# Kernel tuning notes

Measured on AMD Instinct MI355X. Metric: run time of the kernel, lower is better.

The kernel has to match this reference:

```python
import jax, jax.numpy as jnp
import numpy as np

N_NODES = 32768
N_EDGES = 262144
B = 64
FT_IN = 256
HID = 256
HEADS = 4
C = HID // HEADS
FT_OUT = 256
NEG_SLOPE = 0.2


def _lin(k, fi, fo):
    return jax.random.normal(k, (fi, fo), dtype=jnp.float32) / np.sqrt(fi)


def setup_inputs() -> dict:
    key = jax.random.key(0)
    ks = jax.random.split(key, 20)
    x = jax.random.normal(ks[0], (N_NODES, FT_IN), dtype=jnp.float32)
    edge_index = jax.random.randint(ks[1], (2, N_EDGES), 0, N_NODES, dtype=jnp.int64)
    batch = jnp.repeat(jnp.arange(B, dtype=jnp.int64), N_NODES // B)  # sorted segment ids
    return {
        "x": x,
        "edge_index": edge_index,
        "batch": batch,
        "batch_size": B,
        "W1l": _lin(ks[2], FT_IN, HID),
        "W1r": _lin(ks[3], FT_IN, HID),
        "a1": jax.random.normal(ks[4], (HEADS, C), dtype=jnp.float32) / np.sqrt(C),
        "b1": jnp.zeros((HID,), dtype=jnp.float32),
        "W2l": _lin(ks[5], HID, HID),
        "W2r": _lin(ks[6], HID, HID),
        "a2": jax.random.normal(ks[7], (HEADS, C), dtype=jnp.float32) / np.sqrt(C),
        "b2": jnp.zeros((HID,), dtype=jnp.float32),
        "Wm1": _lin(ks[8], HID, 4 * HID),
        "bm1": jnp.zeros((4 * HID,), dtype=jnp.float32),
        "Wm2": _lin(ks[9], 4 * HID, HID),
        "bm2": jnp.zeros((HID,), dtype=jnp.float32),
        "Wf": _lin(ks[10], HID, FT_OUT),
        "bf": jnp.zeros((FT_OUT,), dtype=jnp.float32),
    }


def gatv2_layer(x, src, dst, Wl, Wr, att, bias):
    """PyG GATv2Conv (concat=True, add_self_loops=True, eval-mode dropout)."""
    n = x.shape[0]
    h, c = att.shape
    xl = (x @ Wl).reshape(n, h, c)  # source-side transform (x_j)
    xr = (x @ Wr).reshape(n, h, c)  # target-side transform (x_i)
    loop = jnp.arange(n, dtype=src.dtype)
    s = jnp.concatenate([src, loop])
    d = jnp.concatenate([dst, loop])
    # e_ij = a^T LeakyReLU(Wl x_j + Wr x_i), per head
    e = jax.nn.leaky_relu(xl[s] + xr[d], NEG_SLOPE)  # [E+N, H, C]
    score = jnp.einsum('ehc,hc->eh', e, att)  # [E+N, H]
    # segment softmax over incoming edges of each dst node
    m = jax.ops.segment_max(score, d, num_segments=n)
    ex = jnp.exp(score - m[d])
    denom = jax.ops.segment_sum(ex, d, num_segments=n)
    alpha = ex / denom[d]  # self-loops guarantee denom > 0
    out = jax.ops.segment_sum(alpha[..., None] * xl[s], d, num_segments=n)
    return out.reshape(n, h * c) + bias


def _gelu(x):
    return jax.nn.gelu(x, approximate=False)


def reference(x, edge_index, batch, batch_size,
              W1l, W1r, a1, b1, W2l, W2r, a2, b2,
              Wm1, bm1, Wm2, bm2, Wf, bf):
    src, dst = edge_index[0], edge_index[1]
    h = _gelu(gatv2_layer(x, src, dst, W1l, W1r, a1, b1))
    h = _gelu(gatv2_layer(h, src, dst, W2l, W2r, a2, b2))
    # global mean pool over graphs
    cnt = jax.ops.segment_sum(jnp.ones((h.shape[0],), h.dtype), batch, num_segments=batch_size)
    graph_mean = jax.ops.segment_sum(h, batch, num_segments=batch_size) / cnt[:, None]
    # root node of each graph (node 0 of each contiguous block)
    root = h.reshape(batch_size, -1, h.shape[-1])[:, 0, :]
    z = _gelu(root @ Wm1 + bm1)
    z = _gelu(z @ Wm2 + bm2)
    out = z @ Wf + bf
    return (out, graph_mean)
```

## Files before the change

### kernel.cpp

```cpp
#include <hip/hip_runtime.h>
#include <math.h>

#define NNODES 32768
#define BGRAPH 64
#define NPG 512
#define HID 256

typedef __bf16 bf16x8 __attribute__((ext_vector_type(8)));
typedef float f32x16 __attribute__((ext_vector_type(16)));
typedef unsigned short ushort_t;
typedef unsigned short ushort8v __attribute__((ext_vector_type(8)));
typedef unsigned short ushort4v __attribute__((ext_vector_type(4)));
typedef _Float16 half4v __attribute__((ext_vector_type(4)));

__device__ __forceinline__ float gelu_f(float x) {
  return 0.5f * x * (1.0f + erff(x * 0.70710678118654752440f));
}

__device__ __forceinline__ int swz_off(int r, int k) {
  int kblk = k & ~63;
  int ch = (k >> 3) & 7;
  int slot = ch ^ (r & 7);
  return r * 256 + kblk + (slot << 3) + (k & 7);
}

__device__ __forceinline__ size_t frag_off(int r, int k) {
  return ((size_t)((r >> 5) * 16 + (k >> 4)) << 9) +
         (size_t)(((r & 31) | (((k >> 3) & 1) << 5)) << 3) + (k & 7);
}

__device__ __forceinline__ void gll16(const void* g, void* l) {
  __builtin_amdgcn_global_load_lds(
      (const __attribute__((address_space(1))) unsigned int*)g,
      (__attribute__((address_space(3))) unsigned int*)l, 16, 0, 0);
}

__device__ __forceinline__ float dpp_sum16(float x) {
  int t;
  t = __builtin_amdgcn_update_dpp(0, __builtin_bit_cast(int, x), 0xB1, 0xF, 0xF, true);
  x += __builtin_bit_cast(float, t);
  t = __builtin_amdgcn_update_dpp(0, __builtin_bit_cast(int, x), 0x4E, 0xF, 0xF, true);
  x += __builtin_bit_cast(float, t);
  t = __builtin_amdgcn_update_dpp(0, __builtin_bit_cast(int, x), 0x141, 0xF, 0xF, true);
  x += __builtin_bit_cast(float, t);
  t = __builtin_amdgcn_update_dpp(0, __builtin_bit_cast(int, x), 0x140, 0xF, 0xF, true);
  x += __builtin_bit_cast(float, t);
  return x;
}

__device__ __forceinline__ float wave_sum64(float x) {
  x = dpp_sum16(x);
  x += __shfl_xor(x, 16);
  x += __shfl_xor(x, 32);
  return x;
}

__global__ __launch_bounds__(256) void prep_kernel(
    const int* __restrict__ src, const int* __restrict__ dst, int E,
    int* __restrict__ cnt, ushort_t* __restrict__ col_pad,
    const float* __restrict__ W1l, const float* __restrict__ W1r,
    const float* __restrict__ W2l, const float* __restrict__ W2r,
    ushort_t* __restrict__ B1h, ushort_t* __restrict__ B1l,
    ushort_t* __restrict__ B2h, ushort_t* __restrict__ B2l,
    const float* __restrict__ x,
    ushort_t* __restrict__ Xh, ushort_t* __restrict__ Xl,
    const float* __restrict__ Wm1, const float* __restrict__ Wm2,
    const float* __restrict__ Wf,
    float* __restrict__ W1T, float* __restrict__ W2T, float* __restrict__ WfT) {
  int b = blockIdx.x;
  if (b < 1024) {
    int e = b * 256 + threadIdx.x;
    if (e < E) {
      int d = dst[e];
      int slot = atomicAdd(&cnt[d], 1);
      if (slot < 64) col_pad[(d << 6) | slot] = (ushort_t)src[e];
    }
  } else if (b < 1152) {
    int idx = (b - 1024) * 256 + threadIdx.x;
    int layer = idx >> 14;
    int n = (idx >> 5) & 511;
    int c32 = idx & 31;
    const float* W = layer ? (n < 256 ? W2l : W2r) : (n < 256 ? W1l : W1r);
    int wn = n & 255;
    ushort8v hv, lv;
#pragma unroll
    for (int j = 0; j < 8; ++j) {
      float v = W[(size_t)(c32 * 8 + j) * 256 + wn];
      __bf16 h = (__bf16)v;
      float rem = v - (float)h;
      __bf16 l = (__bf16)rem;
      hv[j] = __builtin_bit_cast(ushort_t, h);
      lv[j] = __builtin_bit_cast(ushort_t, l);
    }
    size_t off = frag_off(n, c32 * 8);
    ushort_t* ho = layer ? B2h : B1h;
    ushort_t* lo = layer ? B2l : B1l;
    *(ushort8v*)(ho + off) = hv;
    *(ushort8v*)(lo + off) = lv;
  } else if (b < 5248) {
    int idx = (b - 1152) * 256 + threadIdx.x;
    int r = idx >> 5;
    int c32 = idx & 31;
    const float* srcp = x + (size_t)r * 256 + c32 * 8;
    float4 v0 = *(const float4*)srcp;
    float4 v1 = *(const float4*)(srcp + 4);
    float vv[8] = {v0.x, v0.y, v0.z, v0.w, v1.x, v1.y, v1.z, v1.w};
    ushort8v hv, lv;
#pragma unroll
    for (int j = 0; j < 8; ++j) {
      __bf16 h = (__bf16)vv[j];
      float rem = vv[j] - (float)h;
      __bf16 l = (__bf16)rem;
      hv[j] = __builtin_bit_cast(ushort_t, h);
      lv[j] = __builtin_bit_cast(ushort_t, l);
    }
    int off = swz_off(r, c32 * 8);
    *(ushort8v*)(Xh + off) = hv;
    *(ushort8v*)(Xl + off) = lv;
  } else if (b < 6272) {
    int idx = (b - 5248) * 256 + threadIdx.x;
    int k = idx & 255, n = idx >> 8;
    W1T[(size_t)n * 256 + k] = Wm1[(size_t)k * 1024 + n];
  } else if (b < 7296) {
    int idx = (b - 6272) * 256 + threadIdx.x;
    int k = idx & 1023, c = idx >> 10;
    W2T[(size_t)c * 1024 + k] = Wm2[(size_t)k * 256 + c];
  } else {
    int idx = (b - 7296) * 256 + threadIdx.x;
    int k = idx & 255, n = idx >> 8;
    WfT[(size_t)n * 256 + k] = Wf[(size_t)k * 256 + n];
  }
}

__global__ __launch_bounds__(256, 3) void gemm_bf16x3(
    const ushort_t* __restrict__ Ahi, const ushort_t* __restrict__ Alo,
    const ushort_t* __restrict__ Bhi, const ushort_t* __restrict__ Blo,
    _Float16* __restrict__ Cl, float* __restrict__ Cr) {
  __shared__ ushort_t lds[2 * 8192];
  int i = blockIdx.x;
  int xcd = i & 7, slot = i >> 3;
  int bm = (xcd * 32 + (slot >> 2)) * 128;
  int bn = (slot & 3) * 128;

  int tid = threadIdx.x;
  int w = tid >> 6, lane = tid & 63;
  int wm0 = (w >> 1) * 64, wn0 = (w & 1) * 64;
  int r = lane & 31, kg = lane >> 5;
  int cb0 = (bn + wn0) >> 5;

  f32x16 acc[2][2];
#pragma unroll
  for (int mf = 0; mf < 2; ++mf)
#pragma unroll
    for (int nf = 0; nf < 2; ++nf)
#pragma unroll
      for (int e = 0; e < 16; ++e) acc[mf][nf][e] = 0.0f;

  for (int kk = 0; kk < 256; kk += 64) {
#pragma unroll
    for (int t = 0; t < 8; ++t) {
      int tile = t >> 2;
      int q = tid + (t & 3) * 256;
      const ushort_t* gsrc = tile ? Alo : Ahi;
      gll16(gsrc + (size_t)(bm + (q >> 3)) * 256 + kk + (q & 7) * 8,
            lds + tile * 8192 + q * 8);
    }
    __syncthreads();

    int kq0 = kk >> 4;
#pragma unroll
    for (int ks = 0; ks < 4; ++ks) {
      int so = (((ks << 1) | kg) ^ (r & 7)) << 3;
      bf16x8 ah[2], al[2], bh[2], bl[2];
#pragma unroll
      for (int mf = 0; mf < 2; ++mf) {
        int rb = (wm0 + mf * 32 + r) * 64 + so;
        ah[mf] = *(const bf16x8*)(lds + rb);
        al[mf] = *(const bf16x8*)(lds + 8192 + rb);
      }
#pragma unroll
      for (int nf = 0; nf < 2; ++nf) {
        size_t o = ((size_t)((cb0 + nf) * 16 + kq0 + ks) << 9) + (lane << 3);
        bh[nf] = *(const bf16x8*)(Bhi + o);
        bl[nf] = *(const bf16x8*)(Blo + o);
      }
#pragma unroll
      for (int mf = 0; mf < 2; ++mf)
#pragma unroll
        for (int nf = 0; nf < 2; ++nf) {
          acc[mf][nf] = __builtin_amdgcn_mfma_f32_32x32x16_bf16(ah[mf], bh[nf], acc[mf][nf], 0, 0, 0);
          acc[mf][nf] = __builtin_amdgcn_mfma_f32_32x32x16_bf16(ah[mf], bl[nf], acc[mf][nf], 0, 0, 0);
          acc[mf][nf] = __builtin_amdgcn_mfma_f32_32x32x16_bf16(al[mf], bh[nf], acc[mf][nf], 0, 0, 0);
        }
    }
    __syncthreads();
  }

#pragma unroll
  for (int mf = 0; mf < 2; ++mf)
#pragma unroll
    for (int nf = 0; nf < 2; ++nf) {
      int colbase = bn + wn0 + nf * 32;
      int cn = (colbase + r) & 255;
#pragma unroll
      for (int g = 0; g < 16; ++g) {
        int row = bm + wm0 + mf * 32 + (g & 3) + ((g >> 2) << 3) + (kg << 2);
        if (colbase < 256)
          Cl[(size_t)row * 256 + cn] = (_Float16)acc[mf][nf][g];
        else
          Cr[(size_t)row * 256 + cn] = acc[mf][nf][g];
      }
    }
}

__global__ __launch_bounds__(256) void gat_agg(const _Float16* __restrict__ xl,
                                               const float* __restrict__ xr,
                                               const float* __restrict__ att,
                                               const float* __restrict__ bias,
                                               const int* __restrict__ cnt,
                                               const ushort_t* __restrict__ col_pad,
                                               ushort_t* __restrict__ hi_out,
                                               ushort_t* __restrict__ lo_out,
                                               _Float16* __restrict__ h2f16,
                                               float* __restrict__ rootbuf) {
  int wave = (int)((blockIdx.x * (size_t)blockDim.x + threadIdx.x) >> 6);
  int lane = threadIdx.x & 63;
  int d = wave;
  int c0 = lane * 4;
  float4 xr4 = *(const float4*)(xr + (size_t)d * HID + c0);
  float4 a4 = *(const float4*)(att + c0);
  int deg = cnt[d];
  deg = deg < 64 ? deg : 64;
  int mycol = (int)col_pad[(d << 6) + lane];

  auto loadrow = [&](int j) -> float4 {
    int s = (j < deg) ? __builtin_amdgcn_readlane(mycol, j) : d;
    half4v hv = *(const half4v*)(xl + (size_t)s * HID + c0);
    return make_float4((float)hv[0], (float)hv[1], (float)hv[2], (float)hv[3]);
  };

  float l = 0.f, A0 = 0.f, A1 = 0.f, A2 = 0.f, A3 = 0.f;
  float4 v = loadrow(0);
  for (int j = 0; j <= deg; ++j) {
    float4 vc = v;
    if (j < deg) v = loadrow(j + 1);
    float t0 = vc.x + xr4.x, t1 = vc.y + xr4.y, t2 = vc.z + xr4.z, t3 = vc.w + xr4.w;
    t0 = fmaf(0.4f, fabsf(t0), 0.6f * t0);
    t1 = fmaf(0.4f, fabsf(t1), 0.6f * t1);
    t2 = fmaf(0.4f, fabsf(t2), 0.6f * t2);
    t3 = fmaf(0.4f, fabsf(t3), 0.6f * t3);
    float sc = a4.x * t0;
    sc = fmaf(a4.y, t1, sc);
    sc = fmaf(a4.z, t2, sc);
    sc = fmaf(a4.w, t3, sc);
    sc = dpp_sum16(sc);
    float p = __expf(sc);
    l += p;
    A0 = fmaf(p, vc.x, A0);
    A1 = fmaf(p, vc.y, A1);
    A2 = fmaf(p, vc.z, A2);
    A3 = fmaf(p, vc.w, A3);
  }

  float inv = 1.0f / l;
  float v0 = gelu_f(fmaf(A0, inv, bias[c0 + 0]));
  float v1 = gelu_f(fmaf(A1, inv, bias[c0 + 1]));
  float v2 = gelu_f(fmaf(A2, inv, bias[c0 + 2]));
  float v3 = gelu_f(fmaf(A3, inv, bias[c0 + 3]));

  if (hi_out) {
    float vv[4] = {v0, v1, v2, v3};
    ushort4v hv, lv;
#pragma unroll
    for (int j = 0; j < 4; ++j) {
      __bf16 h = (__bf16)vv[j];
      float rem = vv[j] - (float)h;
      __bf16 lb = (__bf16)rem;
      hv[j] = __builtin_bit_cast(ushort_t, h);
      lv[j] = __builtin_bit_cast(ushort_t, lb);
    }
    int off = swz_off(d, c0);
    *(ushort4v*)(hi_out + off) = hv;
    *(ushort4v*)(lo_out + off) = lv;
  }
  if (h2f16) {
    half4v o;
    o[0] = (_Float16)v0; o[1] = (_Float16)v1; o[2] = (_Float16)v2; o[3] = (_Float16)v3;
    *(half4v*)(h2f16 + (size_t)d * HID + c0) = o;
    if ((d & (NPG - 1)) == 0)
      *(float4*)(rootbuf + (size_t)(d >> 9) * HID + c0) = make_float4(v0, v1, v2, v3);
  }
}

__global__ __launch_bounds__(1024) void pool_kernel(const _Float16* __restrict__ h2,
                                                    float* __restrict__ gmean) {
  __shared__ float buf[1024];
  int g = blockIdx.x;
  int q = threadIdx.x >> 8;
  int c = threadIdx.x & 255;
  const _Float16* p = h2 + ((size_t)g * NPG + q * 128) * HID + c;
  float s = 0.f;
#pragma unroll 4
  for (int i = 0; i < 128; ++i) s += (float)p[(size_t)i * HID];
  buf[threadIdx.x] = s;
  __syncthreads();
  if (threadIdx.x < 256) {
    float tot = buf[c] + buf[256 + c] + buf[512 + c] + buf[768 + c];
    gmean[(size_t)g * HID + c] = tot * (1.0f / (float)NPG);
  }
}

__global__ __launch_bounds__(256) void head1(const float* __restrict__ root,
                                             const float* __restrict__ W1T,
                                             const float* __restrict__ b1m,
                                             float* __restrict__ z1) {
  int wv = (int)((blockIdx.x * 256 + threadIdx.x) >> 6);
  int lane = threadIdx.x & 63;
  int g = wv >> 10, nx = wv & 1023;
  float4 r = *(const float4*)(root + (size_t)g * 256 + lane * 4);
  float4 w = *(const float4*)(W1T + (size_t)nx * 256 + lane * 4);
  float p = r.x * w.x;
  p = fmaf(r.y, w.y, p);
  p = fmaf(r.z, w.z, p);
  p = fmaf(r.w, w.w, p);
  p = wave_sum64(p);
  if (lane == 0) z1[(size_t)g * 1024 + nx] = gelu_f(p + b1m[nx]);
}

__global__ __launch_bounds__(256) void head2(const float* __restrict__ z1,
                                             const float* __restrict__ W2T,
                                             const float* __restrict__ b2m,
                                             float* __restrict__ z2) {
  int wv = (int)((blockIdx.x * 256 + threadIdx.x) >> 6);
  int lane = threadIdx.x & 63;
  int g = wv >> 8, c = wv & 255;
  const float* zr = z1 + (size_t)g * 1024;
  const float* wr = W2T + (size_t)c * 1024;
  float p = 0.f;
#pragma unroll
  for (int i = 0; i < 4; ++i) {
    float4 a = *(const float4*)(zr + i * 256 + lane * 4);
    float4 w = *(const float4*)(wr + i * 256 + lane * 4);
    p = fmaf(a.x, w.x, p);
    p = fmaf(a.y, w.y, p);
    p = fmaf(a.z, w.z, p);
    p = fmaf(a.w, w.w, p);
  }
  p = wave_sum64(p);
  if (lane == 0) z2[(size_t)g * 256 + c] = gelu_f(p + b2m[c]);
}

__global__ __launch_bounds__(256) void head3(const float* __restrict__ z2,
                                             const float* __restrict__ WfT,
                                             const float* __restrict__ bfm,
                                             float* __restrict__ outp) {
  int wv = (int)((blockIdx.x * 256 + threadIdx.x) >> 6);
  int lane = threadIdx.x & 63;
  int g = wv >> 8, nx = wv & 255;
  float4 a = *(const float4*)(z2 + (size_t)g * 256 + lane * 4);
  float4 w = *(const float4*)(WfT + (size_t)nx * 256 + lane * 4);
  float p = a.x * w.x;
  p = fmaf(a.y, w.y, p);
  p = fmaf(a.z, w.z, p);
  p = fmaf(a.w, w.w, p);
  p = wave_sum64(p);
  if (lane == 0) outp[(size_t)g * 256 + nx] = p + bfm[nx];
}

extern "C" void kernel_launch(void* const* d_in, const int* in_sizes, int n_in,
                              void* d_out, int out_size, void* d_ws, size_t ws_size,
                              hipStream_t stream) {
  const float* x   = (const float*)d_in[0];
  const int* edge  = (const int*)d_in[1];
  const float* W1l = (const float*)d_in[4];
  const float* W1r = (const float*)d_in[5];
  const float* a1  = (const float*)d_in[6];
  const float* b1  = (const float*)d_in[7];
  const float* W2l = (const float*)d_in[8];
  const float* W2r = (const float*)d_in[9];
  const float* a2  = (const float*)d_in[10];
  const float* b2  = (const float*)d_in[11];
  const float* Wm1 = (const float*)d_in[12];
  const float* bm1 = (const float*)d_in[13];
  const float* Wm2 = (const float*)d_in[14];
  const float* bm2 = (const float*)d_in[15];
  const float* Wf  = (const float*)d_in[16];
  const float* bf  = (const float*)d_in[17];
  float* out = (float*)d_out;
  float* gmean = out + BGRAPH * HID;

  const int n = NNODES;
  const int E = in_sizes[1] / 2;
  const int* src = edge;
  const int* dst = edge + E;

  ushort_t* R1h = (ushort_t*)d_ws;
  ushort_t* R1l = R1h + (size_t)n * 256;
  _Float16* h2f16 = (_Float16*)R1h;
  _Float16* xlh = (_Float16*)(R1l + (size_t)n * 256);
  float* xrbuf = (float*)(xlh + (size_t)n * 256);
  float* rootbuf = xrbuf + (size_t)n * 256;
  float* z1 = rootbuf + 64 * 256;
  float* z2 = z1 + 64 * 1024;
  ushort_t* B1h = (ushort_t*)(z2 + 64 * 256);
  ushort_t* B1l = B1h + 512 * 256;
  ushort_t* B2h = B1l + 512 * 256;
  ushort_t* B2l = B2h + 512 * 256;
  int* cnt = (int*)(B2l + 512 * 256);
  ushort_t* col_pad = (ushort_t*)(cnt + n);
  float* W1T = (float*)(col_pad + (size_t)n * 64);
  float* W2T = W1T + 1024 * 256;
  float* WfT = W2T + 256 * 1024;

  hipMemsetAsync(cnt, 0, (size_t)n * sizeof(int), stream);

  prep_kernel<<<7552, 256, 0, stream>>>(
      src, dst, E, cnt, col_pad, W1l, W1r, W2l, W2r,
      B1h, B1l, B2h, B2l, x, R1h, R1l,
      Wm1, Wm2, Wf, W1T, W2T, WfT);

  gemm_bf16x3<<<1024, 256, 0, stream>>>(R1h, R1l, B1h, B1l, xlh, xrbuf);
  gat_agg<<<n / 4, 256, 0, stream>>>(xlh, xrbuf, a1, b1, cnt, col_pad,
                                     R1h, R1l, nullptr, nullptr);
  gemm_bf16x3<<<1024, 256, 0, stream>>>(R1h, R1l, B2h, B2l, xlh, xrbuf);
  gat_agg<<<n / 4, 256, 0, stream>>>(xlh, xrbuf, a2, b2, cnt, col_pad,
                                     nullptr, nullptr, h2f16, rootbuf);

  pool_kernel<<<BGRAPH, 1024, 0, stream>>>(h2f16, gmean);
  head1<<<BGRAPH * 1024 / 4, 256, 0, stream>>>(rootbuf, W1T, bm1, z1);
  head2<<<BGRAPH * 256 / 4, 256, 0, stream>>>(z1, W2T, bm2, z2);
  head3<<<BGRAPH * 256 / 4, 256, 0, stream>>>(z2, WfT, bf, out);
}
```

Baseline: 294.6 us.

## Double-buffer GEMM LDS, fp16 xr, tiled weight transposes, split pool with atomics

```diff
diff --git a/kernel.cpp b/kernel.cpp
--- a/kernel.cpp
+++ b/kernel.cpp
@@ -67,6 +67,7 @@
     const float* __restrict__ Wm1, const float* __restrict__ Wm2,
     const float* __restrict__ Wf,
     float* __restrict__ W1T, float* __restrict__ W2T, float* __restrict__ WfT) {
+  __shared__ float tl[32][33];
   int b = blockIdx.x;
   if (b < 1024) {
     int e = b * 256 + threadIdx.x;
@@ -117,26 +118,39 @@
     int off = swz_off(r, c32 * 8);
     *(ushort8v*)(Xh + off) = hv;
     *(ushort8v*)(Xl + off) = lv;
-  } else if (b < 6272) {
-    int idx = (b - 5248) * 256 + threadIdx.x;
-    int k = idx & 255, n = idx >> 8;
-    W1T[(size_t)n * 256 + k] = Wm1[(size_t)k * 1024 + n];
-  } else if (b < 7296) {
-    int idx = (b - 6272) * 256 + threadIdx.x;
-    int k = idx & 1023, c = idx >> 10;
-    W2T[(size_t)c * 1024 + k] = Wm2[(size_t)k * 256 + c];
   } else {
-    int idx = (b - 7296) * 256 + threadIdx.x;
-    int k = idx & 255, n = idx >> 8;
-    WfT[(size_t)n * 256 + k] = Wf[(size_t)k * 256 + n];
-  }
-}
-
-__global__ __launch_bounds__(256, 3) void gemm_bf16x3(
+    const float* tsrc;
+    float* tdst;
+    int R, C, trow, tcol;
+    if (b < 5504) {
+      int t = b - 5248;
+      tsrc = Wm1; tdst = W1T; R = 256; C = 1024;
+      trow = (t >> 5) << 5; tcol = (t & 31) << 5;
+    } else if (b < 5760) {
+      int t = b - 5504;
+      tsrc = Wm2; tdst = W2T; R = 1024; C = 256;
+      trow = (t >> 3) << 5; tcol = (t & 7) << 5;
+    } else {
+      int t = b - 5760;
+      tsrc = Wf; tdst = WfT; R = 256; C = 256;
+      trow = (t >> 3) << 5; tcol = (t & 7) << 5;
+    }
+    int lc = threadIdx.x & 31, lr = threadIdx.x >> 5;
+#pragma unroll
+    for (int p = 0; p < 4; ++p)
+      tl[p * 8 + lr][lc] = tsrc[(size_t)(trow + p * 8 + lr) * C + tcol + lc];
+    __syncthreads();
+#pragma unroll
+    for (int p = 0; p < 4; ++p)
+      tdst[(size_t)(tcol + p * 8 + lr) * R + trow + lc] = tl[lc][p * 8 + lr];
+  }
+}
+
+__global__ __launch_bounds__(256, 2) void gemm_bf16x3(
     const ushort_t* __restrict__ Ahi, const ushort_t* __restrict__ Alo,
     const ushort_t* __restrict__ Bhi, const ushort_t* __restrict__ Blo,
-    _Float16* __restrict__ Cl, float* __restrict__ Cr) {
-  __shared__ ushort_t lds[2 * 8192];
+    _Float16* __restrict__ Cl, _Float16* __restrict__ Cr) {
+  __shared__ ushort_t lds[2][2 * 8192];
   int i = blockIdx.x;
   int xcd = i & 7, slot = i >> 3;
   int bm = (xcd * 32 + (slot >> 2)) * 128;
@@ -148,26 +162,34 @@
   int r = lane & 31, kg = lane >> 5;
   int cb0 = (bn + wn0) >> 5;
 
-  f32x16 acc[2][2];
-#pragma unroll
-  for (int mf = 0; mf < 2; ++mf)
-#pragma unroll
-    for (int nf = 0; nf < 2; ++nf)
-#pragma unroll
-      for (int e = 0; e < 16; ++e) acc[mf][nf][e] = 0.0f;
-
-  for (int kk = 0; kk < 256; kk += 64) {
+  auto stage = [&](int kk, int buf) {
 #pragma unroll
     for (int t = 0; t < 8; ++t) {
       int tile = t >> 2;
       int q = tid + (t & 3) * 256;
       const ushort_t* gsrc = tile ? Alo : Ahi;
       gll16(gsrc + (size_t)(bm + (q >> 3)) * 256 + kk + (q & 7) * 8,
-            lds + tile * 8192 + q * 8);
-    }
-    __syncthreads();
-
-    int kq0 = kk >> 4;
+            &lds[buf][tile * 8192 + q * 8]);
+    }
+  };
+
+  f32x16 acc[2][2];
+#pragma unroll
+  for (int mf = 0; mf < 2; ++mf)
+#pragma unroll
+    for (int nf = 0; nf < 2; ++nf)
+#pragma unroll
+      for (int e = 0; e < 16; ++e) acc[mf][nf][e] = 0.0f;
+
+  stage(0, 0);
+  __syncthreads();
+
+#pragma unroll
+  for (int k4 = 0; k4 < 4; ++k4) {
+    int buf = k4 & 1;
+    if (k4 < 3) stage((k4 + 1) * 64, buf ^ 1);
+
+    int kq0 = k4 * 4;
 #pragma unroll
     for (int ks = 0; ks < 4; ++ks) {
       int so = (((ks << 1) | kg) ^ (r & 7)) << 3;
@@ -175,8 +197,8 @@
 #pragma unroll
       for (int mf = 0; mf < 2; ++mf) {
         int rb = (wm0 + mf * 32 + r) * 64 + so;
-        ah[mf] = *(const bf16x8*)(lds + rb);
-        al[mf] = *(const bf16x8*)(lds + 8192 + rb);
+        ah[mf] = *(const bf16x8*)(&lds[buf][rb]);
+        al[mf] = *(const bf16x8*)(&lds[buf][8192 + rb]);
       }
 #pragma unroll
       for (int nf = 0; nf < 2; ++nf) {
@@ -202,19 +224,17 @@
     for (int nf = 0; nf < 2; ++nf) {
       int colbase = bn + wn0 + nf * 32;
       int cn = (colbase + r) & 255;
+      _Float16* Cbase = (colbase < 256) ? Cl : Cr;
 #pragma unroll
       for (int g = 0; g < 16; ++g) {
         int row = bm + wm0 + mf * 32 + (g & 3) + ((g >> 2) << 3) + (kg << 2);
-        if (colbase < 256)
-          Cl[(size_t)row * 256 + cn] = (_Float16)acc[mf][nf][g];
-        else
-          Cr[(size_t)row * 256 + cn] = acc[mf][nf][g];
+        Cbase[(size_t)row * 256 + cn] = (_Float16)acc[mf][nf][g];
       }
     }
 }
 
 __global__ __launch_bounds__(256) void gat_agg(const _Float16* __restrict__ xl,
-                                               const float* __restrict__ xr,
+                                               const _Float16* __restrict__ xr,
                                                const float* __restrict__ att,
                                                const float* __restrict__ bias,
                                                const int* __restrict__ cnt,
@@ -227,7 +247,8 @@
   int lane = threadIdx.x & 63;
   int d = wave;
   int c0 = lane * 4;
-  float4 xr4 = *(const float4*)(xr + (size_t)d * HID + c0);
+  half4v xrh = *(const half4v*)(xr + (size_t)d * HID + c0);
+  float4 xr4 = make_float4((float)xrh[0], (float)xrh[1], (float)xrh[2], (float)xrh[3]);
   float4 a4 = *(const float4*)(att + c0);
   int deg = cnt[d];
   deg = deg < 64 ? deg : 64;
@@ -292,22 +313,16 @@
   }
 }
 
-__global__ __launch_bounds__(1024) void pool_kernel(const _Float16* __restrict__ h2,
-                                                    float* __restrict__ gmean) {
-  __shared__ float buf[1024];
-  int g = blockIdx.x;
-  int q = threadIdx.x >> 8;
-  int c = threadIdx.x & 255;
-  const _Float16* p = h2 + ((size_t)g * NPG + q * 128) * HID + c;
+__global__ __launch_bounds__(256) void pool_kernel(const _Float16* __restrict__ h2,
+                                                   float* __restrict__ gmean) {
+  int g = blockIdx.x >> 3;
+  int q = blockIdx.x & 7;
+  int c = threadIdx.x;
+  const _Float16* p = h2 + ((size_t)g * NPG + q * 64) * HID + c;
   float s = 0.f;
 #pragma unroll 4
-  for (int i = 0; i < 128; ++i) s += (float)p[(size_t)i * HID];
-  buf[threadIdx.x] = s;
-  __syncthreads();
-  if (threadIdx.x < 256) {
-    float tot = buf[c] + buf[256 + c] + buf[512 + c] + buf[768 + c];
-    gmean[(size_t)g * HID + c] = tot * (1.0f / (float)NPG);
-  }
+  for (int i = 0; i < 64; ++i) s += (float)p[(size_t)i * HID];
+  atomicAdd(&gmean[(size_t)g * HID + c], s * (1.0f / (float)NPG));
 }
 
 __global__ __launch_bounds__(256) void head1(const float* __restrict__ root,
@@ -398,8 +413,8 @@
   ushort_t* R1l = R1h + (size_t)n * 256;
   _Float16* h2f16 = (_Float16*)R1h;
   _Float16* xlh = (_Float16*)(R1l + (size_t)n * 256);
-  float* xrbuf = (float*)(xlh + (size_t)n * 256);
-  float* rootbuf = xrbuf + (size_t)n * 256;
+  _Float16* xrh = xlh + (size_t)n * 256;
+  float* rootbuf = (float*)(xrh + (size_t)n * 256);
   float* z1 = rootbuf + 64 * 256;
   float* z2 = z1 + 64 * 1024;
   ushort_t* B1h = (ushort_t*)(z2 + 64 * 256);
@@ -413,20 +428,21 @@
   float* WfT = W2T + 256 * 1024;
 
   hipMemsetAsync(cnt, 0, (size_t)n * sizeof(int), stream);
-
-  prep_kernel<<<7552, 256, 0, stream>>>(
+  hipMemsetAsync(gmean, 0, (size_t)BGRAPH * HID * sizeof(float), stream);
+
+  prep_kernel<<<5824, 256, 0, stream>>>(
       src, dst, E, cnt, col_pad, W1l, W1r, W2l, W2r,
       B1h, B1l, B2h, B2l, x, R1h, R1l,
       Wm1, Wm2, Wf, W1T, W2T, WfT);
 
-  gemm_bf16x3<<<1024, 256, 0, stream>>>(R1h, R1l, B1h, B1l, xlh, xrbuf);
-  gat_agg<<<n / 4, 256, 0, stream>>>(xlh, xrbuf, a1, b1, cnt, col_pad,
+  gemm_bf16x3<<<1024, 256, 0, stream>>>(R1h, R1l, B1h, B1l, xlh, xrh);
+  gat_agg<<<n / 4, 256, 0, stream>>>(xlh, xrh, a1, b1, cnt, col_pad,
                                      R1h, R1l, nullptr, nullptr);
-  gemm_bf16x3<<<1024, 256, 0, stream>>>(R1h, R1l, B2h, B2l, xlh, xrbuf);
-  gat_agg<<<n / 4, 256, 0, stream>>>(xlh, xrbuf, a2, b2, cnt, col_pad,
+  gemm_bf16x3<<<1024, 256, 0, stream>>>(R1h, R1l, B2h, B2l, xlh, xrh);
+  gat_agg<<<n / 4, 256, 0, stream>>>(xlh, xrh, a2, b2, cnt, col_pad,
                                      nullptr, nullptr, h2f16, rootbuf);
 
-  pool_kernel<<<BGRAPH, 1024, 0, stream>>>(h2f16, gmean);
+  pool_kernel<<<BGRAPH * 8, 256, 0, stream>>>(h2f16, gmean);
   head1<<<BGRAPH * 1024 / 4, 256, 0, stream>>>(rootbuf, W1T, bm1, z1);
   head2<<<BGRAPH * 256 / 4, 256, 0, stream>>>(z1, W2T, bm2, z2);
   head3<<<BGRAPH * 256 / 4, 256, 0, stream>>>(z2, WfT, bf, out);
```

Result: faster. 283.6 us (-3.7%).
